# Performance work log

Hardware: AMD Instinct MI355X
Metric: run time of the kernel (lower is better)

Reference implementation:

```python
import jax, jax.numpy as jnp
import numpy as np

EPS = 1e-06
K = 4          # hc_mult
D = 2048       # hidden_size
SINKHORN_ITERS = 20


def setup_inputs() -> dict:
    key = jax.random.key(0)
    k1, k2, k3 = jax.random.split(key, 3)
    B, S = 2, 4096
    x = jax.random.normal(k1, (B, S, K, D), dtype=jnp.float32)
    out = jax.random.normal(k2, (B, S, D), dtype=jnp.float32)
    out_dim = (2 + K) * K  # 24
    # matches nn.init.normal_(std=1/sqrt(K*D))
    W = jax.random.normal(k3, (out_dim, K * D), dtype=jnp.float32) / np.sqrt(K * D)
    scale = jnp.ones((3,), dtype=jnp.float32)
    base = jnp.zeros((out_dim,), dtype=jnp.float32)
    return {"x": x, "out": out, "W": W, "scale": scale, "base": base}


def _sinkhorn(m, n_iters=SINKHORN_ITERS, eps=EPS):
    # one priming column normalization, then (n_iters-1) row/col cycles
    m = m / (jnp.sum(m, axis=-2, keepdims=True) + eps)
    for _ in range(max(n_iters - 1, 0)):
        m = m / (jnp.sum(m, axis=-1, keepdims=True) + eps)
        m = m / (jnp.sum(m, axis=-2, keepdims=True) + eps)
    return m


def reference(x, out, W, scale, base):
    out_dtype = x.dtype
    # --- _packed_logits: flatten K streams, RMS-normalize, project (fp32) ---
    flat = x.reshape(*x.shape[:-2], K * D).astype(jnp.float32)      # [B,S,K*D]
    rsqrt = jax.lax.rsqrt(jnp.mean(flat * flat, axis=-1, keepdims=True) + EPS)
    logits = jnp.einsum('bsf,of->bso', flat * rsqrt, W)             # [B,S,24]
    # --- compute_weights: split into pre/post/comb ---
    pre_logit = logits[..., :K] * scale[0] + base[:K]
    post_logit = logits[..., K:2 * K] * scale[1] + base[K:2 * K]
    comb_logit = (logits[..., 2 * K:].reshape(*logits.shape[:-1], K, K) * scale[2]
                  + base[2 * K:].reshape(K, K))
    pre = jax.nn.sigmoid(pre_logit) + EPS                           # [B,S,K]
    post = 2.0 * jax.nn.sigmoid(post_logit)                         # [B,S,K]
    comb = jax.nn.softmax(comb_logit, axis=-1) + EPS                # [B,S,K,K]
    comb = _sinkhorn(comb)                                          # doubly-stochastic
    pre = pre.astype(out_dtype)
    post = post.astype(out_dtype)
    comb = comb.astype(out_dtype)
    # --- collapse: K streams -> 1 via pre weights ---
    collapsed = jnp.sum(pre[..., None] * x, axis=-2)                # [B,S,D]
    # --- expand: write sub-block output back to K streams ---
    write = post[..., None] * out[..., None, :]                     # [B,S,K,D]
    mix = jnp.einsum('bshk,bskd->bshd', comb, x)                    # [B,S,K,D]
    y = write + mix
    return (y, collapsed)
```

## Files before the change

### kernel.cpp

```cpp
#include <hip/hip_runtime.h>


#define EPS 1e-6f
constexpr int D_ = 2048, KD = 8192, NOUT = 24;
constexpr int NTOK = 8192;
constexpr int TPB = 512;
constexpr int TOKS = 3;
constexpr int NBLK = (NTOK + TOKS - 1) / TOKS;

typedef _Float16 h2 __attribute__((ext_vector_type(2)));

static __device__ __forceinline__ unsigned int pk2(float a, float b) {
    h2 h; h.x = (_Float16)a; h.y = (_Float16)b;
    return __builtin_bit_cast(unsigned int, h);
}

static __device__ __forceinline__ float dot2(unsigned int w, unsigned int x, float c) {
#if __has_builtin(__builtin_amdgcn_fdot2)
    return __builtin_amdgcn_fdot2(__builtin_bit_cast(h2, w),
                                  __builtin_bit_cast(h2, x), c, false);
#else
    h2 hw = __builtin_bit_cast(h2, w), hx = __builtin_bit_cast(h2, x);
    return c + (float)hw.x * (float)hx.x + (float)hw.y * (float)hx.y;
#endif
}

static __device__ __forceinline__ float frcp(float v) {
#if __has_builtin(__builtin_amdgcn_rcpf)
    return __builtin_amdgcn_rcpf(v);
#else
    return 1.f / v;
#endif
}

__global__ void conv_w_kernel(const float* __restrict__ W, unsigned int* __restrict__ Wh) {
    int g = blockIdx.x * blockDim.x + threadIdx.x;
    const float* src = W + (size_t)g * 8;
    float4 a = *reinterpret_cast<const float4*>(src);
    float4 b = *reinterpret_cast<const float4*>(src + 4);
    uint4 u;
    u.x = pk2(a.x, a.y); u.y = pk2(a.z, a.w);
    u.z = pk2(b.x, b.y); u.w = pk2(b.z, b.w);
    *reinterpret_cast<uint4*>(Wh + (size_t)g * 4) = u;
}

__global__ __launch_bounds__(TPB) void hypermix_kernel(
    const float* __restrict__ x, const float* __restrict__ outp,
    const unsigned int* __restrict__ Wh,
    const float* __restrict__ scale, const float* __restrict__ base,
    float* __restrict__ y, float* __restrict__ coll)
{
    const int t = threadIdx.x;
    const int w = t >> 6, lane = t & 63;
    const size_t gt0 = (size_t)blockIdx.x * TOKS;
    const size_t tks0 = gt0;
    const size_t tks1 = (gt0 + 1 < NTOK) ? gt0 + 1 : NTOK - 1;
    const size_t tks2 = (gt0 + 2 < NTOK) ? gt0 + 2 : NTOK - 1;

    __shared__ unsigned int xh[TOKS][KD / 2];
    __shared__ float os[TOKS][D_];
    __shared__ float ssred[TOKS][8];
    __shared__ float lg[TOKS][24];
    __shared__ float wts[TOKS][24];

    {
        const float* xb0 = x + tks0 * KD + t * 4;
        const float* xb1 = x + tks1 * KD + t * 4;
        const float* xb2 = x + tks2 * KD + t * 4;
        float4 a0[4], a1[4], a2[4];
#pragma unroll
        for (int i = 0; i < 4; ++i) a0[i] = *reinterpret_cast<const float4*>(xb0 + i * 2048);
#pragma unroll
        for (int i = 0; i < 4; ++i) a1[i] = *reinterpret_cast<const float4*>(xb1 + i * 2048);
#pragma unroll
        for (int i = 0; i < 4; ++i) a2[i] = *reinterpret_cast<const float4*>(xb2 + i * 2048);
        float4 o0 = *reinterpret_cast<const float4*>(outp + tks0 * D_ + t * 4);
        float4 o1 = *reinterpret_cast<const float4*>(outp + tks1 * D_ + t * 4);
        float4 o2 = *reinterpret_cast<const float4*>(outp + tks2 * D_ + t * 4);

        float ss0 = 0.f, ss1 = 0.f, ss2 = 0.f;
#pragma unroll
        for (int i = 0; i < 4; ++i) {
            ss0 += a0[i].x * a0[i].x + a0[i].y * a0[i].y + a0[i].z * a0[i].z + a0[i].w * a0[i].w;
            uint2 p; p.x = pk2(a0[i].x, a0[i].y); p.y = pk2(a0[i].z, a0[i].w);
            *reinterpret_cast<uint2*>(&xh[0][i * 1024 + t * 2]) = p;
        }
#pragma unroll
        for (int i = 0; i < 4; ++i) {
            ss1 += a1[i].x * a1[i].x + a1[i].y * a1[i].y + a1[i].z * a1[i].z + a1[i].w * a1[i].w;
            uint2 p; p.x = pk2(a1[i].x, a1[i].y); p.y = pk2(a1[i].z, a1[i].w);
            *reinterpret_cast<uint2*>(&xh[1][i * 1024 + t * 2]) = p;
        }
#pragma unroll
        for (int i = 0; i < 4; ++i) {
            ss2 += a2[i].x * a2[i].x + a2[i].y * a2[i].y + a2[i].z * a2[i].z + a2[i].w * a2[i].w;
            uint2 p; p.x = pk2(a2[i].x, a2[i].y); p.y = pk2(a2[i].z, a2[i].w);
            *reinterpret_cast<uint2*>(&xh[2][i * 1024 + t * 2]) = p;
        }
        *reinterpret_cast<float4*>(&os[0][t * 4]) = o0;
        *reinterpret_cast<float4*>(&os[1][t * 4]) = o1;
        *reinterpret_cast<float4*>(&os[2][t * 4]) = o2;

#pragma unroll
        for (int m = 1; m < 64; m <<= 1) {
            ss0 += __shfl_xor(ss0, m, 64);
            ss1 += __shfl_xor(ss1, m, 64);
            ss2 += __shfl_xor(ss2, m, 64);
        }
        if (lane == 0) { ssred[0][w] = ss0; ssred[1][w] = ss1; ssred[2][w] = ss2; }
    }
    __syncthreads();

    {
        const int r0 = w * 3;
        float acc[3][TOKS];
#pragma unroll
        for (int j = 0; j < 3; ++j)
#pragma unroll
            for (int tt = 0; tt < TOKS; ++tt) acc[j][tt] = 0.f;

#pragma unroll 2
        for (int it = 0; it < 16; ++it) {
            const int gi = it * 64 + lane;
            uint4 xv0 = *reinterpret_cast<const uint4*>(&xh[0][gi * 4]);
            uint4 xv1 = *reinterpret_cast<const uint4*>(&xh[1][gi * 4]);
            uint4 xv2 = *reinterpret_cast<const uint4*>(&xh[2][gi * 4]);
#pragma unroll
            for (int j = 0; j < 3; ++j) {
                uint4 wv = *reinterpret_cast<const uint4*>(
                    Wh + ((size_t)(r0 + j) * 4096 + gi * 4));
                acc[j][0] = dot2(wv.x, xv0.x, acc[j][0]);
                acc[j][0] = dot2(wv.y, xv0.y, acc[j][0]);
                acc[j][0] = dot2(wv.z, xv0.z, acc[j][0]);
                acc[j][0] = dot2(wv.w, xv0.w, acc[j][0]);
                acc[j][1] = dot2(wv.x, xv1.x, acc[j][1]);
                acc[j][1] = dot2(wv.y, xv1.y, acc[j][1]);
                acc[j][1] = dot2(wv.z, xv1.z, acc[j][1]);
                acc[j][1] = dot2(wv.w, xv1.w, acc[j][1]);
                acc[j][2] = dot2(wv.x, xv2.x, acc[j][2]);
                acc[j][2] = dot2(wv.y, xv2.y, acc[j][2]);
                acc[j][2] = dot2(wv.z, xv2.z, acc[j][2]);
                acc[j][2] = dot2(wv.w, xv2.w, acc[j][2]);
            }
        }
#pragma unroll
        for (int j = 0; j < 3; ++j)
#pragma unroll
            for (int tt = 0; tt < TOKS; ++tt) {
                float v = acc[j][tt];
#pragma unroll
                for (int m = 1; m < 64; m <<= 1) v += __shfl_xor(v, m, 64);
                if (lane == 0) lg[tt][r0 + j] = v;
            }
    }
    __syncthreads();

    if (t < TOKS && gt0 + t < NTOK) {
        float ss = ssred[t][0] + ssred[t][1] + ssred[t][2] + ssred[t][3]
                 + ssred[t][4] + ssred[t][5] + ssred[t][6] + ssred[t][7];
        float rms = rsqrtf(ss * (1.f / 8192.f) + EPS);
        float s0 = scale[0], s1 = scale[1], s2 = scale[2];
        float l[24];
#pragma unroll
        for (int i = 0; i < 24; ++i) l[i] = lg[t][i];
#pragma unroll
        for (int k = 0; k < 4; ++k) {
            float z0 = l[k] * rms * s0 + base[k];
            wts[t][k] = frcp(1.f + __expf(-z0)) + EPS;
            float z1 = l[4 + k] * rms * s1 + base[4 + k];
            wts[t][4 + k] = 2.f * frcp(1.f + __expf(-z1));
        }
        float p[16];
#pragma unroll
        for (int h = 0; h < 4; ++h) {
            float c0 = l[8 + h * 4 + 0] * rms * s2 + base[8 + h * 4 + 0];
            float c1 = l[8 + h * 4 + 1] * rms * s2 + base[8 + h * 4 + 1];
            float c2 = l[8 + h * 4 + 2] * rms * s2 + base[8 + h * 4 + 2];
            float c3 = l[8 + h * 4 + 3] * rms * s2 + base[8 + h * 4 + 3];
            float mx = fmaxf(fmaxf(c0, c1), fmaxf(c2, c3));
            float e0 = __expf(c0 - mx), e1 = __expf(c1 - mx);
            float e2 = __expf(c2 - mx), e3 = __expf(c3 - mx);
            float inv = frcp(e0 + e1 + e2 + e3);
            p[h * 4 + 0] = e0 * inv + EPS; p[h * 4 + 1] = e1 * inv + EPS;
            p[h * 4 + 2] = e2 * inv + EPS; p[h * 4 + 3] = e3 * inv + EPS;
        }
#pragma unroll
        for (int k = 0; k < 4; ++k) {
            float inv = frcp(p[k] + p[4 + k] + p[8 + k] + p[12 + k] + EPS);
            p[k] *= inv; p[4 + k] *= inv; p[8 + k] *= inv; p[12 + k] *= inv;
        }
#pragma unroll 1
        for (int itn = 0; itn < 19; ++itn) {
#pragma unroll
            for (int h = 0; h < 4; ++h) {
                float inv = frcp(p[h * 4] + p[h * 4 + 1] + p[h * 4 + 2] + p[h * 4 + 3] + EPS);
                p[h * 4] *= inv; p[h * 4 + 1] *= inv; p[h * 4 + 2] *= inv; p[h * 4 + 3] *= inv;
            }
#pragma unroll
            for (int k = 0; k < 4; ++k) {
                float inv = frcp(p[k] + p[4 + k] + p[8 + k] + p[12 + k] + EPS);
                p[k] *= inv; p[4 + k] *= inv; p[8 + k] *= inv; p[12 + k] *= inv;
            }
        }
#pragma unroll
        for (int i = 0; i < 16; ++i) wts[t][8 + i] = p[i];
    }
    __syncthreads();

#pragma unroll 1
    for (int tt = 0; tt < TOKS; ++tt) {
        if (gt0 + tt >= NTOK) continue;
        float pre[4], post[4], cmb[4][4];
#pragma unroll
        for (int k = 0; k < 4; ++k) { pre[k] = wts[tt][k]; post[k] = wts[tt][4 + k]; }
#pragma unroll
        for (int h = 0; h < 4; ++h)
#pragma unroll
            for (int k = 0; k < 4; ++k) cmb[h][k] = wts[tt][8 + h * 4 + k];

        const int d = t * 4;
        float xk[4][4];
#pragma unroll
        for (int k = 0; k < 4; ++k) {
            uint2 pq = *reinterpret_cast<const uint2*>(&xh[tt][k * 1024 + t * 2]);
            h2 h0 = __builtin_bit_cast(h2, pq.x), h1 = __builtin_bit_cast(h2, pq.y);
            xk[k][0] = (float)h0.x; xk[k][1] = (float)h0.y;
            xk[k][2] = (float)h1.x; xk[k][3] = (float)h1.y;
        }
        float4 ov = *reinterpret_cast<const float4*>(&os[tt][t * 4]);
        float* yb = y + (gt0 + tt) * KD;
        float* cb = coll + (gt0 + tt) * D_;
        float cv[4], yv[4];
#pragma unroll
        for (int e = 0; e < 4; ++e)
            cv[e] = pre[0] * xk[0][e] + pre[1] * xk[1][e]
                  + pre[2] * xk[2][e] + pre[3] * xk[3][e];
        *reinterpret_cast<float4*>(cb + d) = make_float4(cv[0], cv[1], cv[2], cv[3]);
        const float oe[4] = {ov.x, ov.y, ov.z, ov.w};
#pragma unroll
        for (int h = 0; h < 4; ++h) {
#pragma unroll
            for (int e = 0; e < 4; ++e)
                yv[e] = post[h] * oe[e] + cmb[h][0] * xk[0][e] + cmb[h][1] * xk[1][e]
                      + cmb[h][2] * xk[2][e] + cmb[h][3] * xk[3][e];
            *reinterpret_cast<float4*>(yb + h * D_ + d) =
                make_float4(yv[0], yv[1], yv[2], yv[3]);
        }
    }
}

extern "C" void kernel_launch(void* const* d_in, const int* in_sizes, int n_in,
                              void* d_out, int out_size, void* d_ws, size_t ws_size,
                              hipStream_t stream) {
    const float* x     = (const float*)d_in[0];
    const float* outp  = (const float*)d_in[1];
    const float* W     = (const float*)d_in[2];
    const float* scale = (const float*)d_in[3];
    const float* base  = (const float*)d_in[4];
    float* y    = (float*)d_out;
    float* coll = y + (size_t)NTOK * KD;

    unsigned int* Wh = (unsigned int*)d_ws;
    conv_w_kernel<<<NOUT * KD / 8 / 256, 256, 0, stream>>>(W, Wh);
    hypermix_kernel<<<NBLK, TPB, 0, stream>>>(x, outp, Wh, scale, base, y, coll);
}
```

Baseline: 180.6 us.

## Stage x via global_load_lds in fp32, two tokens per block, fuse packing into dot loop

Loads x directly from global memory into LDS in fp32 with async global_load_lds instead of going through registers and packing to fp16. The fp16 packing and the sum of squares now happen inside the projection loop, and W is re-laid out to match. Tokens per block drop from 3 to 2, and the collapse/expand step reads the full-precision fp32 x from LDS. The `out` load is deferred to the final phase. LDS use rises to 64KB per block, which may limit occupancy, and only one wave computes the RMS sum.

After: 188.4 us. 1.04x slower.

```diff
diff --git a/kernel.cpp b/kernel.cpp
--- a/kernel.cpp
+++ b/kernel.cpp
@@ -5,14 +5,19 @@
 constexpr int D_ = 2048, KD = 8192, NOUT = 24;
 constexpr int NTOK = 8192;
 constexpr int TPB = 512;
-constexpr int TOKS = 3;
-constexpr int NBLK = (NTOK + TOKS - 1) / TOKS;
+constexpr int TOKS = 2;
+constexpr int NBLK = NTOK / TOKS;
 
 typedef _Float16 h2 __attribute__((ext_vector_type(2)));
 
 static __device__ __forceinline__ unsigned int pk2(float a, float b) {
+#if __has_builtin(__builtin_amdgcn_cvt_pkrtz)
+    auto r = __builtin_amdgcn_cvt_pkrtz(a, b);
+    return __builtin_bit_cast(unsigned int, r);
+#else
     h2 h; h.x = (_Float16)a; h.y = (_Float16)b;
     return __builtin_bit_cast(unsigned int, h);
+#endif
 }
 
 static __device__ __forceinline__ float dot2(unsigned int w, unsigned int x, float c) {
@@ -33,132 +38,106 @@
 #endif
 }
 
-__global__ void conv_w_kernel(const float* __restrict__ W, unsigned int* __restrict__ Wh) {
+__global__ void conv_w_kernel(const float* __restrict__ W, uint4* __restrict__ Wh4) {
     int g = blockIdx.x * blockDim.x + threadIdx.x;
-    const float* src = W + (size_t)g * 8;
+    int o = g >> 10, rem = g & 1023;
+    int it = rem >> 6, lane = rem & 63;
+    const float* src = W + o * KD + it * 512 + lane * 4;
     float4 a = *reinterpret_cast<const float4*>(src);
-    float4 b = *reinterpret_cast<const float4*>(src + 4);
+    float4 b = *reinterpret_cast<const float4*>(src + 256);
     uint4 u;
     u.x = pk2(a.x, a.y); u.y = pk2(a.z, a.w);
     u.z = pk2(b.x, b.y); u.w = pk2(b.z, b.w);
-    *reinterpret_cast<uint4*>(Wh + (size_t)g * 4) = u;
+    Wh4[g] = u;
 }
 
 __global__ __launch_bounds__(TPB) void hypermix_kernel(
     const float* __restrict__ x, const float* __restrict__ outp,
-    const unsigned int* __restrict__ Wh,
+    const uint4* __restrict__ Wh4,
     const float* __restrict__ scale, const float* __restrict__ base,
     float* __restrict__ y, float* __restrict__ coll)
 {
     const int t = threadIdx.x;
     const int w = t >> 6, lane = t & 63;
     const size_t gt0 = (size_t)blockIdx.x * TOKS;
-    const size_t tks0 = gt0;
-    const size_t tks1 = (gt0 + 1 < NTOK) ? gt0 + 1 : NTOK - 1;
-    const size_t tks2 = (gt0 + 2 < NTOK) ? gt0 + 2 : NTOK - 1;
-
-    __shared__ unsigned int xh[TOKS][KD / 2];
-    __shared__ float os[TOKS][D_];
-    __shared__ float ssred[TOKS][8];
-    __shared__ float lg[TOKS][24];
-    __shared__ float wts[TOKS][24];
-
-    {
-        const float* xb0 = x + tks0 * KD + t * 4;
-        const float* xb1 = x + tks1 * KD + t * 4;
-        const float* xb2 = x + tks2 * KD + t * 4;
-        float4 a0[4], a1[4], a2[4];
-#pragma unroll
-        for (int i = 0; i < 4; ++i) a0[i] = *reinterpret_cast<const float4*>(xb0 + i * 2048);
-#pragma unroll
-        for (int i = 0; i < 4; ++i) a1[i] = *reinterpret_cast<const float4*>(xb1 + i * 2048);
-#pragma unroll
-        for (int i = 0; i < 4; ++i) a2[i] = *reinterpret_cast<const float4*>(xb2 + i * 2048);
-        float4 o0 = *reinterpret_cast<const float4*>(outp + tks0 * D_ + t * 4);
-        float4 o1 = *reinterpret_cast<const float4*>(outp + tks1 * D_ + t * 4);
-        float4 o2 = *reinterpret_cast<const float4*>(outp + tks2 * D_ + t * 4);
-
-        float ss0 = 0.f, ss1 = 0.f, ss2 = 0.f;
-#pragma unroll
-        for (int i = 0; i < 4; ++i) {
-            ss0 += a0[i].x * a0[i].x + a0[i].y * a0[i].y + a0[i].z * a0[i].z + a0[i].w * a0[i].w;
-            uint2 p; p.x = pk2(a0[i].x, a0[i].y); p.y = pk2(a0[i].z, a0[i].w);
-            *reinterpret_cast<uint2*>(&xh[0][i * 1024 + t * 2]) = p;
-        }
-#pragma unroll
-        for (int i = 0; i < 4; ++i) {
-            ss1 += a1[i].x * a1[i].x + a1[i].y * a1[i].y + a1[i].z * a1[i].z + a1[i].w * a1[i].w;
-            uint2 p; p.x = pk2(a1[i].x, a1[i].y); p.y = pk2(a1[i].z, a1[i].w);
-            *reinterpret_cast<uint2*>(&xh[1][i * 1024 + t * 2]) = p;
-        }
-#pragma unroll
-        for (int i = 0; i < 4; ++i) {
-            ss2 += a2[i].x * a2[i].x + a2[i].y * a2[i].y + a2[i].z * a2[i].z + a2[i].w * a2[i].w;
-            uint2 p; p.x = pk2(a2[i].x, a2[i].y); p.y = pk2(a2[i].z, a2[i].w);
-            *reinterpret_cast<uint2*>(&xh[2][i * 1024 + t * 2]) = p;
-        }
-        *reinterpret_cast<float4*>(&os[0][t * 4]) = o0;
-        *reinterpret_cast<float4*>(&os[1][t * 4]) = o1;
-        *reinterpret_cast<float4*>(&os[2][t * 4]) = o2;
-
-#pragma unroll
-        for (int m = 1; m < 64; m <<= 1) {
-            ss0 += __shfl_xor(ss0, m, 64);
-            ss1 += __shfl_xor(ss1, m, 64);
-            ss2 += __shfl_xor(ss2, m, 64);
-        }
-        if (lane == 0) { ssred[0][w] = ss0; ssred[1][w] = ss1; ssred[2][w] = ss2; }
+
+    __shared__ float stage[TOKS][KD];
+    __shared__ float ssv[TOKS];
+    __shared__ float lg[TOKS][NOUT];
+    __shared__ float wts[TOKS][NOUT];
+
+#pragma unroll
+    for (int tt = 0; tt < TOKS; ++tt) {
+        const float* gsrc = x + (gt0 + tt) * KD + t * 4;
+#pragma unroll
+        for (int i = 0; i < 4; ++i)
+            __builtin_amdgcn_global_load_lds(
+                (const __attribute__((address_space(1))) unsigned int*)(gsrc + i * 2048),
+                (__attribute__((address_space(3))) unsigned int*)(&stage[tt][i * 2048 + t * 4]),
+                16, 0, 0);
     }
     __syncthreads();
 
     {
         const int r0 = w * 3;
-        float acc[3][TOKS];
-#pragma unroll
-        for (int j = 0; j < 3; ++j)
-#pragma unroll
-            for (int tt = 0; tt < TOKS; ++tt) acc[j][tt] = 0.f;
+        float acc[3][2];
+#pragma unroll
+        for (int j = 0; j < 3; ++j) { acc[j][0] = 0.f; acc[j][1] = 0.f; }
+        float ss0 = 0.f, ss1 = 0.f;
 
 #pragma unroll 2
         for (int it = 0; it < 16; ++it) {
-            const int gi = it * 64 + lane;
-            uint4 xv0 = *reinterpret_cast<const uint4*>(&xh[0][gi * 4]);
-            uint4 xv1 = *reinterpret_cast<const uint4*>(&xh[1][gi * 4]);
-            uint4 xv2 = *reinterpret_cast<const uint4*>(&xh[2][gi * 4]);
+            const int f = it * 512 + lane * 4;
+            float4 x00 = *reinterpret_cast<const float4*>(&stage[0][f]);
+            float4 x01 = *reinterpret_cast<const float4*>(&stage[0][f + 256]);
+            float4 x10 = *reinterpret_cast<const float4*>(&stage[1][f]);
+            float4 x11 = *reinterpret_cast<const float4*>(&stage[1][f + 256]);
+            if (w == 7) {
+                ss0 += x00.x * x00.x + x00.y * x00.y + x00.z * x00.z + x00.w * x00.w
+                     + x01.x * x01.x + x01.y * x01.y + x01.z * x01.z + x01.w * x01.w;
+                ss1 += x10.x * x10.x + x10.y * x10.y + x10.z * x10.z + x10.w * x10.w
+                     + x11.x * x11.x + x11.y * x11.y + x11.z * x11.z + x11.w * x11.w;
+            }
+            unsigned int p00 = pk2(x00.x, x00.y), p01 = pk2(x00.z, x00.w);
+            unsigned int p02 = pk2(x01.x, x01.y), p03 = pk2(x01.z, x01.w);
+            unsigned int p10 = pk2(x10.x, x10.y), p11 = pk2(x10.z, x10.w);
+            unsigned int p12 = pk2(x11.x, x11.y), p13 = pk2(x11.z, x11.w);
 #pragma unroll
             for (int j = 0; j < 3; ++j) {
-                uint4 wv = *reinterpret_cast<const uint4*>(
-                    Wh + ((size_t)(r0 + j) * 4096 + gi * 4));
-                acc[j][0] = dot2(wv.x, xv0.x, acc[j][0]);
-                acc[j][0] = dot2(wv.y, xv0.y, acc[j][0]);
-                acc[j][0] = dot2(wv.z, xv0.z, acc[j][0]);
-                acc[j][0] = dot2(wv.w, xv0.w, acc[j][0]);
-                acc[j][1] = dot2(wv.x, xv1.x, acc[j][1]);
-                acc[j][1] = dot2(wv.y, xv1.y, acc[j][1]);
-                acc[j][1] = dot2(wv.z, xv1.z, acc[j][1]);
-                acc[j][1] = dot2(wv.w, xv1.w, acc[j][1]);
-                acc[j][2] = dot2(wv.x, xv2.x, acc[j][2]);
-                acc[j][2] = dot2(wv.y, xv2.y, acc[j][2]);
-                acc[j][2] = dot2(wv.z, xv2.z, acc[j][2]);
-                acc[j][2] = dot2(wv.w, xv2.w, acc[j][2]);
-            }
-        }
-#pragma unroll
-        for (int j = 0; j < 3; ++j)
-#pragma unroll
-            for (int tt = 0; tt < TOKS; ++tt) {
-                float v = acc[j][tt];
-#pragma unroll
-                for (int m = 1; m < 64; m <<= 1) v += __shfl_xor(v, m, 64);
-                if (lane == 0) lg[tt][r0 + j] = v;
-            }
+                uint4 wv = Wh4[(size_t)(r0 + j) * 1024 + it * 64 + lane];
+                acc[j][0] = dot2(wv.x, p00, acc[j][0]);
+                acc[j][0] = dot2(wv.y, p01, acc[j][0]);
+                acc[j][0] = dot2(wv.z, p02, acc[j][0]);
+                acc[j][0] = dot2(wv.w, p03, acc[j][0]);
+                acc[j][1] = dot2(wv.x, p10, acc[j][1]);
+                acc[j][1] = dot2(wv.y, p11, acc[j][1]);
+                acc[j][1] = dot2(wv.z, p12, acc[j][1]);
+                acc[j][1] = dot2(wv.w, p13, acc[j][1]);
+            }
+        }
+#pragma unroll
+        for (int j = 0; j < 3; ++j) {
+            float v0 = acc[j][0], v1 = acc[j][1];
+#pragma unroll
+            for (int m = 1; m < 64; m <<= 1) {
+                v0 += __shfl_xor(v0, m, 64);
+                v1 += __shfl_xor(v1, m, 64);
+            }
+            if (lane == 0) { lg[0][r0 + j] = v0; lg[1][r0 + j] = v1; }
+        }
+        if (w == 7) {
+#pragma unroll
+            for (int m = 1; m < 64; m <<= 1) {
+                ss0 += __shfl_xor(ss0, m, 64);
+                ss1 += __shfl_xor(ss1, m, 64);
+            }
+            if (lane == 0) { ssv[0] = ss0; ssv[1] = ss1; }
+        }
     }
     __syncthreads();
 
-    if (t < TOKS && gt0 + t < NTOK) {
-        float ss = ssred[t][0] + ssred[t][1] + ssred[t][2] + ssred[t][3]
-                 + ssred[t][4] + ssred[t][5] + ssred[t][6] + ssred[t][7];
-        float rms = rsqrtf(ss * (1.f / 8192.f) + EPS);
+    if (t < TOKS) {
+        float rms = rsqrtf(ssv[t] * (1.f / 8192.f) + EPS);
         float s0 = scale[0], s1 = scale[1], s2 = scale[2];
         float l[24];
 #pragma unroll
@@ -181,8 +160,8 @@
             float e0 = __expf(c0 - mx), e1 = __expf(c1 - mx);
             float e2 = __expf(c2 - mx), e3 = __expf(c3 - mx);
             float inv = frcp(e0 + e1 + e2 + e3);
-            p[h * 4 + 0] = e0 * inv + EPS; p[h * 4 + 1] = e1 * inv + EPS;
-            p[h * 4 + 2] = e2 * inv + EPS; p[h * 4 + 3] = e3 * inv + EPS;
+            p[0 + h * 4] = e0 * inv + EPS; p[1 + h * 4] = e1 * inv + EPS;
+            p[2 + h * 4] = e2 * inv + EPS; p[3 + h * 4] = e3 * inv + EPS;
         }
 #pragma unroll
         for (int k = 0; k < 4; ++k) {
@@ -207,44 +186,49 @@
     }
     __syncthreads();
 
-#pragma unroll 1
-    for (int tt = 0; tt < TOKS; ++tt) {
-        if (gt0 + tt >= NTOK) continue;
-        float pre[4], post[4], cmb[4][4];
-#pragma unroll
-        for (int k = 0; k < 4; ++k) { pre[k] = wts[tt][k]; post[k] = wts[tt][4 + k]; }
-#pragma unroll
-        for (int h = 0; h < 4; ++h)
-#pragma unroll
-            for (int k = 0; k < 4; ++k) cmb[h][k] = wts[tt][8 + h * 4 + k];
-
-        const int d = t * 4;
-        float xk[4][4];
-#pragma unroll
-        for (int k = 0; k < 4; ++k) {
-            uint2 pq = *reinterpret_cast<const uint2*>(&xh[tt][k * 1024 + t * 2]);
-            h2 h0 = __builtin_bit_cast(h2, pq.x), h1 = __builtin_bit_cast(h2, pq.y);
-            xk[k][0] = (float)h0.x; xk[k][1] = (float)h0.y;
-            xk[k][2] = (float)h1.x; xk[k][3] = (float)h1.y;
-        }
-        float4 ov = *reinterpret_cast<const float4*>(&os[tt][t * 4]);
-        float* yb = y + (gt0 + tt) * KD;
-        float* cb = coll + (gt0 + tt) * D_;
-        float cv[4], yv[4];
-#pragma unroll
-        for (int e = 0; e < 4; ++e)
-            cv[e] = pre[0] * xk[0][e] + pre[1] * xk[1][e]
-                  + pre[2] * xk[2][e] + pre[3] * xk[3][e];
-        *reinterpret_cast<float4*>(cb + d) = make_float4(cv[0], cv[1], cv[2], cv[3]);
-        const float oe[4] = {ov.x, ov.y, ov.z, ov.w};
-#pragma unroll
-        for (int h = 0; h < 4; ++h) {
+    {
+        float4 ov0 = *reinterpret_cast<const float4*>(outp + gt0 * D_ + t * 4);
+        float4 ov1 = *reinterpret_cast<const float4*>(outp + (gt0 + 1) * D_ + t * 4);
+#pragma unroll
+        for (int tt = 0; tt < TOKS; ++tt) {
+            float pre[4], post[4], cmb[4][4];
+#pragma unroll
+            for (int k = 0; k < 4; ++k) { pre[k] = wts[tt][k]; post[k] = wts[tt][4 + k]; }
+#pragma unroll
+            for (int h = 0; h < 4; ++h)
+#pragma unroll
+                for (int k = 0; k < 4; ++k) cmb[h][k] = wts[tt][8 + h * 4 + k];
+
+            const int d = t * 4;
+            float4 xk[4];
+#pragma unroll
+            for (int k = 0; k < 4; ++k)
+                xk[k] = *reinterpret_cast<const float4*>(&stage[tt][k * D_ + d]);
+            const float xe[4][4] = {
+                {xk[0].x, xk[0].y, xk[0].z, xk[0].w},
+                {xk[1].x, xk[1].y, xk[1].z, xk[1].w},
+                {xk[2].x, xk[2].y, xk[2].z, xk[2].w},
+                {xk[3].x, xk[3].y, xk[3].z, xk[3].w}};
+            float4 ov = tt ? ov1 : ov0;
+            const float oe[4] = {ov.x, ov.y, ov.z, ov.w};
+
+            float* yb = y + (gt0 + tt) * KD;
+            float* cb = coll + (gt0 + tt) * D_;
+            float cv[4], yv[4];
 #pragma unroll
             for (int e = 0; e < 4; ++e)
-                yv[e] = post[h] * oe[e] + cmb[h][0] * xk[0][e] + cmb[h][1] * xk[1][e]
-                      + cmb[h][2] * xk[2][e] + cmb[h][3] * xk[3][e];
-            *reinterpret_cast<float4*>(yb + h * D_ + d) =
-                make_float4(yv[0], yv[1], yv[2], yv[3]);
+                cv[e] = pre[0] * xe[0][e] + pre[1] * xe[1][e]
+                      + pre[2] * xe[2][e] + pre[3] * xe[3][e];
+            *reinterpret_cast<float4*>(cb + d) = make_float4(cv[0], cv[1], cv[2], cv[3]);
+#pragma unroll
+            for (int h = 0; h < 4; ++h) {
+#pragma unroll
+                for (int e = 0; e < 4; ++e)
+                    yv[e] = post[h] * oe[e] + cmb[h][0] * xe[0][e] + cmb[h][1] * xe[1][e]
+                          + cmb[h][2] * xe[2][e] + cmb[h][3] * xe[3][e];
+                *reinterpret_cast<float4*>(yb + h * D_ + d) =
+                    make_float4(yv[0], yv[1], yv[2], yv[3]);
+            }
         }
     }
 }
@@ -260,7 +244,7 @@
     float* y    = (float*)d_out;
     float* coll = y + (size_t)NTOK * KD;
 
-    unsigned int* Wh = (unsigned int*)d_ws;
-    conv_w_kernel<<<NOUT * KD / 8 / 256, 256, 0, stream>>>(W, Wh);
-    hypermix_kernel<<<NBLK, TPB, 0, stream>>>(x, outp, Wh, scale, base, y, coll);
-}
+    uint4* Wh4 = (uint4*)d_ws;
+    conv_w_kernel<<<NOUT * KD / 8 / 256, 256, 0, stream>>>(W, Wh4);
+    hypermix_kernel<<<NBLK, TPB, 0, stream>>>(x, outp, Wh4, scale, base, y, coll);
+}
```
